# Kernel tuning notes

Hardware: AMD Instinct MI355X
Metric: run time of the kernel (lower is better)

Reference implementation:

```python
import jax, jax.numpy as jnp
import numpy as np

EMBED_DIM = 384
HEADS = 6
HEAD_DIM = EMBED_DIM // HEADS
WINDOW = 64


def setup_inputs() -> dict:
    key = jax.random.key(0)
    ks = jax.random.split(key, 5)
    B, T = 128, 256
    s_attn = 1.0 / np.sqrt(EMBED_DIM)
    x = jax.random.normal(ks[0], (B, T, EMBED_DIM), dtype=jnp.float32)
    W_attn = jax.random.normal(ks[1], (EMBED_DIM, 3 * EMBED_DIM), dtype=jnp.float32) * s_attn
    b_attn = jax.random.normal(ks[2], (3 * EMBED_DIM,), dtype=jnp.float32) * 0.02
    W_proj = jax.random.normal(ks[3], (EMBED_DIM, EMBED_DIM), dtype=jnp.float32) * s_attn
    b_proj = jax.random.normal(ks[4], (EMBED_DIM,), dtype=jnp.float32) * 0.02
    return {"x": x, "W_attn": W_attn, "b_attn": b_attn, "W_proj": W_proj, "b_proj": b_proj}


def reference(x, W_attn, b_attn, W_proj, b_proj):
    B, T, C = x.shape
    qkv = x @ W_attn + b_attn  # [B,T,3C]
    q, k, v = jnp.split(qkv, 3, axis=-1)
    # [B, H, T, hd]
    q = q.reshape(B, T, HEADS, HEAD_DIM).transpose(0, 2, 1, 3)
    k = k.reshape(B, T, HEADS, HEAD_DIM).transpose(0, 2, 1, 3)
    v = v.reshape(B, T, HEADS, HEAD_DIM).transpose(0, 2, 1, 3)
    scale = 1.0 / np.sqrt(HEAD_DIM).astype(np.float32)
    att = jnp.einsum('bhqd,bhkd->bhqk', q, k) * scale
    i = jnp.arange(T)
    causal = i[:, None] >= i[None, :]
    local = jnp.abs(i[:, None] - i[None, :]) <= WINDOW
    mask = (causal & local)[None, None, :, :]
    att = jnp.where(mask, att, -jnp.inf)
    att = jax.nn.softmax(att, axis=-1)
    y = jnp.einsum('bhqk,bhkd->bhqd', att, v)
    y = y.transpose(0, 2, 1, 3).reshape(B, T, C)
    return y @ W_proj + b_proj
```

## Files before the change

kernel.cpp:

```cpp
#include <hip/hip_runtime.h>

#define B_SZ   128
#define T_SEQ  256
#define C_DIM  384
#define HEADS  6
#define HD     64
#define WIN    64

typedef __bf16 bf16x8 __attribute__((ext_vector_type(8)));
typedef float  f32x4  __attribute__((ext_vector_type(4)));

typedef __attribute__((address_space(3))) void lds_void;
typedef __attribute__((address_space(1))) void gbl_void;

__device__ __forceinline__ unsigned short f2bf(float f) {
  unsigned u = __float_as_uint(f);
  u += 0x7FFFu + ((u >> 16) & 1u);
  return (unsigned short)(u >> 16);
}

__global__ __launch_bounds__(256) void convert_f32_bf16(
    const float* __restrict__ in, unsigned short* __restrict__ out, int n4) {
  int i = blockIdx.x * blockDim.x + threadIdx.x;
  if (i < n4) {
    float4 v = ((const float4*)in)[i];
    ushort4 o;
    o.x = f2bf(v.x); o.y = f2bf(v.y); o.z = f2bf(v.z); o.w = f2bf(v.w);
    ((ushort4*)out)[i] = o;
  }
}

__global__ __launch_bounds__(256) void transpose_convert(
    const float* __restrict__ in, unsigned short* __restrict__ out,
    int K, int N) {
  __shared__ float tile[32][33];
  const int gx = blockIdx.x * 32;
  const int gy = blockIdx.y * 32;
  const int tx = threadIdx.x;
  const int ty = threadIdx.y;
#pragma unroll
  for (int r = ty; r < 32; r += 8)
    tile[r][tx] = in[(size_t)(gy + r) * N + gx + tx];
  __syncthreads();
#pragma unroll
  for (int r = ty; r < 32; r += 8)
    out[(size_t)(gx + r) * K + gy + tx] = f2bf(tile[tx][r]);
}

template <bool OUT_BF16>
__global__ __launch_bounds__(256, 2) void gemm_mfma_bf16(
    const unsigned short* __restrict__ A,
    const unsigned short* __restrict__ Bt,
    const float* __restrict__ bias,
    void* __restrict__ Cv, int M, int N, int K, int tiles_n) {
  __shared__ __attribute__((aligned(16))) char smem_raw[48 * 1024];
  unsigned short* As = (unsigned short*)smem_raw;
  unsigned short* Bs = As + 256 * 64;
  float* ep = (float*)smem_raw;

  const int t    = threadIdx.x;
  const int lane = t & 63;
  const int w    = t >> 6;

  const unsigned id    = blockIdx.x;
  const unsigned remap = (id & 7u) * (gridDim.x >> 3) + (id >> 3);
  const int by = remap / (unsigned)tiles_n;
  const int bx = remap % (unsigned)tiles_n;
  const int m0 = by * 256;
  const int n0 = bx * 128;

  const int lrow = lane >> 3;
  const int lcol = lane & 7;
  const int schunk = lcol ^ lrow;

  f32x4 acc[4][8];
#pragma unroll
  for (int i = 0; i < 4; ++i)
#pragma unroll
    for (int j = 0; j < 8; ++j) acc[i][j] = (f32x4){0.f, 0.f, 0.f, 0.f};

  const int mfrag = lane & 15;
  const int quad  = lane >> 4;
  const int sw    = mfrag & 7;

  for (int k0 = 0; k0 < K; k0 += 64) {
#pragma unroll
    for (int i = 0; i < 8; ++i) {
      const int inst = w * 8 + i;
      const int r = inst * 8 + lrow;
      const unsigned short* ga = A + (size_t)(m0 + r) * K + k0 + schunk * 8;
      __builtin_amdgcn_global_load_lds((const gbl_void*)ga,
                                       (lds_void*)(As + inst * 512), 16, 0, 0);
    }
#pragma unroll
    for (int i = 0; i < 4; ++i) {
      const int inst = w * 4 + i;
      const int r = inst * 8 + lrow;
      const unsigned short* gb = Bt + (size_t)(n0 + r) * K + k0 + schunk * 8;
      __builtin_amdgcn_global_load_lds((const gbl_void*)gb,
                                       (lds_void*)(Bs + inst * 512), 16, 0, 0);
    }
    __syncthreads();

#pragma unroll
    for (int ks = 0; ks < 64; ks += 32) {
      const int cp = (((ks >> 3) + quad) ^ sw) << 3;
      bf16x8 af[4], bfr[8];
#pragma unroll
      for (int mt = 0; mt < 4; ++mt)
        af[mt] = *(const bf16x8*)(As + (size_t)(w * 64 + mt * 16 + mfrag) * 64 + cp);
#pragma unroll
      for (int nt = 0; nt < 8; ++nt)
        bfr[nt] = *(const bf16x8*)(Bs + (size_t)(nt * 16 + mfrag) * 64 + cp);
#pragma unroll
      for (int mt = 0; mt < 4; ++mt)
#pragma unroll
        for (int nt = 0; nt < 8; ++nt)
          acc[mt][nt] = __builtin_amdgcn_mfma_f32_16x16x32_bf16(
              af[mt], bfr[nt], acc[mt][nt], 0, 0, 0);
    }
    __syncthreads();
  }

  float bv[8];
#pragma unroll
  for (int nt = 0; nt < 8; ++nt) bv[nt] = bias[n0 + nt * 16 + mfrag];

#pragma unroll
  for (int p = 0; p < 4; ++p) {
    if (p) __syncthreads();
    if (w == p) {
#pragma unroll
      for (int mt = 0; mt < 4; ++mt)
#pragma unroll
        for (int nt = 0; nt < 8; ++nt)
#pragma unroll
          for (int r = 0; r < 4; ++r)
            ep[(mt * 16 + quad * 4 + r) * 132 + nt * 16 + mfrag] =
                acc[mt][nt][r] + bv[nt];
    }
    __syncthreads();
#pragma unroll
    for (int cc = 0; cc < 8; ++cc) {
      const int chunk = cc * 256 + t;
      const int row = chunk >> 5;
      const int c4  = chunk & 31;
      f32x4 v = *(const f32x4*)(ep + row * 132 + c4 * 4);
      const int grow = m0 + p * 64 + row;
      const int gcol = n0 + c4 * 4;
      if (OUT_BF16) {
        ushort4 o;
        o.x = f2bf(v[0]); o.y = f2bf(v[1]); o.z = f2bf(v[2]); o.w = f2bf(v[3]);
        *(ushort4*)((unsigned short*)Cv + (size_t)grow * N + gcol) = o;
      } else {
        *(f32x4*)((float*)Cv + (size_t)grow * N + gcol) = v;
      }
    }
  }
}

#define PSTR 68
__global__ __launch_bounds__(256) void attn_mfma(
    const unsigned short* __restrict__ qkv, unsigned short* __restrict__ y) {
  __shared__ unsigned short Qs[64 * 64];
  __shared__ unsigned short Ks[64 * 64];
  __shared__ unsigned short Vt[64 * 64];
  __shared__ float Pw[4][16 * PSTR];

  const unsigned id  = blockIdx.x;
  const unsigned bid = (id & 7u) * (gridDim.x >> 3) + (id >> 3);
  const int qt  = bid & 3;
  const int h   = (bid >> 2) % HEADS;
  const int b   = bid / (4 * HEADS);
  const int t   = threadIdx.x;
  const int lane = t & 63;
  const int w    = t >> 6;
  const int quad = lane >> 4;
  const int m16  = lane & 15;
  const int sw   = m16 & 7;

  const size_t rowbase = (size_t)b * T_SEQ * (3 * C_DIM);
  const int qoff = h * HD;
  const int koff = C_DIM + h * HD;
  const int voff = 2 * C_DIM + h * HD;
  const int qg0  = qt * 64;

  const int lrow = lane >> 3;
  const int lcol = lane & 7;
  const int schunk = lcol ^ lrow;

#pragma unroll
  for (int i = 0; i < 2; ++i) {
    const int inst = w * 2 + i;
    const int r = inst * 8 + lrow;
    const unsigned short* ga =
        qkv + rowbase + (size_t)(qg0 + r) * (3 * C_DIM) + qoff + schunk * 8;
    __builtin_amdgcn_global_load_lds((const gbl_void*)ga,
                                     (lds_void*)(Qs + inst * 512), 16, 0, 0);
  }

  float m_r[4], l_r[4];
  f32x4 yacc[4];
#pragma unroll
  for (int r = 0; r < 4; ++r) { m_r[r] = -1e30f; l_r[r] = 0.f; }
#pragma unroll
  for (int dt = 0; dt < 4; ++dt) yacc[dt] = (f32x4){0.f, 0.f, 0.f, 0.f};

  const int nchunks  = (qt == 0) ? 1 : 2;
  const int kb_first = (qt == 0) ? 0 : (qg0 - 64);
  const int qrow_base = qg0 + w * 16 + quad * 4;

  for (int ch = 0; ch < nchunks; ++ch) {
    const int kb = kb_first + ch * 64;

    __syncthreads();

#pragma unroll
    for (int i = 0; i < 2; ++i) {
      const int inst = w * 2 + i;
      const int r = inst * 8 + lrow;
      const unsigned short* ga =
          qkv + rowbase + (size_t)(kb + r) * (3 * C_DIM) + koff + schunk * 8;
      __builtin_amdgcn_global_load_lds((const gbl_void*)ga,
                                       (lds_void*)(Ks + inst * 512), 16, 0, 0);
    }
    {
      const int vkey = t & 63;
      const int kc = vkey >> 3, ke = vkey & 7;
      const int vd0  = (t >> 6) * 16;
      const unsigned short* gv =
          qkv + rowbase + (size_t)(kb + vkey) * (3 * C_DIM) + voff + vd0;
#pragma unroll
      for (int u = 0; u < 4; ++u) {
        ushort4 vv = *(const ushort4*)(gv + u * 4);
#pragma unroll
        for (int jj = 0; jj < 4; ++jj) {
          const int d = vd0 + u * 4 + jj;
          const unsigned short val =
              (jj == 0) ? vv.x : (jj == 1) ? vv.y : (jj == 2) ? vv.z : vv.w;
          Vt[d * 64 + ((kc ^ (d & 7)) << 3) + ke] = val;
        }
      }
    }
    __syncthreads();

    f32x4 sacc[4];
#pragma unroll
    for (int nt = 0; nt < 4; ++nt) sacc[nt] = (f32x4){0.f, 0.f, 0.f, 0.f};
#pragma unroll
    for (int ks = 0; ks < 64; ks += 32) {
      const int cp = (((ks >> 3) + quad) ^ sw) << 3;
      bf16x8 aq = *(const bf16x8*)(Qs + (size_t)(w * 16 + m16) * 64 + cp);
#pragma unroll
      for (int nt = 0; nt < 4; ++nt) {
        bf16x8 kf = *(const bf16x8*)(Ks + (size_t)(nt * 16 + m16) * 64 + cp);
        sacc[nt] = __builtin_amdgcn_mfma_f32_16x16x32_bf16(aq, kf, sacc[nt], 0, 0, 0);
      }
    }

    float mc[4] = {-1e30f, -1e30f, -1e30f, -1e30f};
#pragma unroll
    for (int nt = 0; nt < 4; ++nt) {
      const int kg = kb + nt * 16 + m16;
#pragma unroll
      for (int r = 0; r < 4; ++r) {
        const int qg = qrow_base + r;
        const bool valid = (kg <= qg) && (qg - kg <= WIN);
        const float sv = valid ? (sacc[nt][r] * 0.125f) : -1e30f;
        sacc[nt][r] = sv;
        mc[r] = fmaxf(mc[r], sv);
      }
    }
#pragma unroll
    for (int r = 0; r < 4; ++r) {
#pragma unroll
      for (int x = 1; x <= 8; x <<= 1) mc[r] = fmaxf(mc[r], __shfl_xor(mc[r], x));
    }

#pragma unroll
    for (int r = 0; r < 4; ++r) {
      const float mn    = fmaxf(m_r[r], mc[r]);
      const float alpha = __expf(m_r[r] - mn);
      m_r[r] = mn;
      l_r[r] *= alpha;
#pragma unroll
      for (int dt = 0; dt < 4; ++dt) yacc[dt][r] *= alpha;
      float ls = 0.f;
#pragma unroll
      for (int nt = 0; nt < 4; ++nt) {
        const float p = __expf(sacc[nt][r] - mn);
        sacc[nt][r] = p;
        ls += p;
      }
#pragma unroll
      for (int x = 1; x <= 8; x <<= 1) ls += __shfl_xor(ls, x);
      l_r[r] += ls;
    }

#pragma unroll
    for (int nt = 0; nt < 4; ++nt)
#pragma unroll
      for (int r = 0; r < 4; ++r)
        Pw[w][(quad * 4 + r) * PSTR + nt * 16 + m16] = sacc[nt][r];

#pragma unroll
    for (int ks = 0; ks < 64; ks += 32) {
      f32x4 pa = *(const f32x4*)(&Pw[w][m16 * PSTR + ks + quad * 8]);
      f32x4 pb = *(const f32x4*)(&Pw[w][m16 * PSTR + ks + quad * 8 + 4]);
      bf16x8 ap;
#pragma unroll
      for (int j = 0; j < 4; ++j) {
        ap[j]     = (__bf16)pa[j];
        ap[4 + j] = (__bf16)pb[j];
      }
      const int cp = (((ks >> 3) + quad) ^ sw) << 3;
#pragma unroll
      for (int dt = 0; dt < 4; ++dt) {
        bf16x8 vf = *(const bf16x8*)(Vt + (size_t)(dt * 16 + m16) * 64 + cp);
        yacc[dt] = __builtin_amdgcn_mfma_f32_16x16x32_bf16(ap, vf, yacc[dt], 0, 0, 0);
      }
    }
  }

  float* epy = &Pw[0][0];
  float inv[4];
#pragma unroll
  for (int r = 0; r < 4; ++r) inv[r] = 1.f / l_r[r];
#pragma unroll
  for (int dt = 0; dt < 4; ++dt)
#pragma unroll
    for (int r = 0; r < 4; ++r)
      epy[(w * 16 + quad * 4 + r) * PSTR + dt * 16 + m16] = yacc[dt][r] * inv[r];
  __syncthreads();
#pragma unroll
  for (int cc = 0; cc < 4; ++cc) {
    const int chunk = cc * 256 + t;
    const int row = chunk >> 4;
    const int c4  = chunk & 15;
    f32x4 v = *(const f32x4*)(epy + row * PSTR + c4 * 4);
    ushort4 o;
    o.x = f2bf(v[0]); o.y = f2bf(v[1]); o.z = f2bf(v[2]); o.w = f2bf(v[3]);
    *(ushort4*)(y + (size_t)(b * T_SEQ + qg0 + row) * C_DIM + h * HD + c4 * 4) = o;
  }
}

extern "C" void kernel_launch(void* const* d_in, const int* in_sizes, int n_in,
                              void* d_out, int out_size, void* d_ws, size_t ws_size,
                              hipStream_t stream) {
  const float* x      = (const float*)d_in[0];
  const float* W_attn = (const float*)d_in[1];
  const float* b_attn = (const float*)d_in[2];
  const float* W_proj = (const float*)d_in[3];
  const float* b_proj = (const float*)d_in[4];
  float* out = (float*)d_out;

  const int M = B_SZ * T_SEQ;

  unsigned short* qkv_b = (unsigned short*)d_ws;
  unsigned short* y_b   = qkv_b + (size_t)M * (3 * C_DIM);
  unsigned short* x_b   = y_b   + (size_t)M * C_DIM;
  unsigned short* Wa_t  = x_b   + (size_t)M * C_DIM;
  unsigned short* Wp_t  = Wa_t  + (size_t)(3 * C_DIM) * C_DIM;

  {
    int n4 = M * C_DIM / 4;
    convert_f32_bf16<<<n4 / 256, 256, 0, stream>>>(x, x_b, n4);
    transpose_convert<<<dim3((3 * C_DIM) / 32, C_DIM / 32), dim3(32, 8), 0, stream>>>(
        W_attn, Wa_t, C_DIM, 3 * C_DIM);
    transpose_convert<<<dim3(C_DIM / 32, C_DIM / 32), dim3(32, 8), 0, stream>>>(
        W_proj, Wp_t, C_DIM, C_DIM);
  }

  gemm_mfma_bf16<true><<<dim3(9 * (M / 256)), 256, 0, stream>>>(
      x_b, Wa_t, b_attn, qkv_b, M, 3 * C_DIM, C_DIM, 9);

  attn_mfma<<<dim3(B_SZ * HEADS * (T_SEQ / 64)), 256, 0, stream>>>(qkv_b, y_b);

  gemm_mfma_bf16<false><<<dim3(3 * (M / 256)), 256, 0, stream>>>(
      y_b, Wp_t, b_proj, out, M, C_DIM, C_DIM, 3);
}
```

Before: 210.9 us.

## Double-buffer GEMM LDS tiles with smaller 128x128 blocks and higher occupancy

Restructures the bf16 MFMA GEMM from 256x128 tiles with a 64-wide K step to 128x128 tiles with a 32-wide K step. Global-to-LDS loads for the next K slice are issued while the current slice is computed, and warps are arranged 2x2. Smaller tiles and less LDS allow four blocks per CU and more blocks overall, at the cost of lower per-block operand reuse and more loop iterations.

```diff
diff --git a/kernel.cpp b/kernel.cpp
--- a/kernel.cpp
+++ b/kernel.cpp
@@ -48,95 +48,105 @@
 }
 
 template <bool OUT_BF16>
-__global__ __launch_bounds__(256, 2) void gemm_mfma_bf16(
+__global__ __launch_bounds__(256, 4) void gemm_mfma_bf16(
     const unsigned short* __restrict__ A,
     const unsigned short* __restrict__ Bt,
     const float* __restrict__ bias,
     void* __restrict__ Cv, int M, int N, int K, int tiles_n) {
-  __shared__ __attribute__((aligned(16))) char smem_raw[48 * 1024];
-  unsigned short* As = (unsigned short*)smem_raw;
-  unsigned short* Bs = As + 256 * 64;
+  __shared__ __attribute__((aligned(16))) char smem_raw[64 * 132 * 4];
+  unsigned short* As0 = (unsigned short*)smem_raw;
+  unsigned short* Bs0 = As0 + 128 * 32;
+  unsigned short* As1 = Bs0 + 128 * 32;
+  unsigned short* Bs1 = As1 + 128 * 32;
   float* ep = (float*)smem_raw;
 
   const int t    = threadIdx.x;
   const int lane = t & 63;
   const int w    = t >> 6;
+  const int wr   = w >> 1;
+  const int wc   = w & 1;
 
   const unsigned id    = blockIdx.x;
   const unsigned remap = (id & 7u) * (gridDim.x >> 3) + (id >> 3);
   const int by = remap / (unsigned)tiles_n;
   const int bx = remap % (unsigned)tiles_n;
-  const int m0 = by * 256;
+  const int m0 = by * 128;
   const int n0 = bx * 128;
 
-  const int lrow = lane >> 3;
-  const int lcol = lane & 7;
-  const int schunk = lcol ^ lrow;
-
-  f32x4 acc[4][8];
+  const int lrow = lane >> 2;
+  const int lcol = lane & 3;
+  const int sc   = lcol ^ ((lrow >> 1) & 3);
+
+  const int m16  = lane & 15;
+  const int quad = lane >> 4;
+  const int cp   = (quad ^ ((m16 >> 1) & 3)) << 3;
+
+  f32x4 acc[4][4];
 #pragma unroll
   for (int i = 0; i < 4; ++i)
 #pragma unroll
-    for (int j = 0; j < 8; ++j) acc[i][j] = (f32x4){0.f, 0.f, 0.f, 0.f};
-
-  const int mfrag = lane & 15;
-  const int quad  = lane >> 4;
-  const int sw    = mfrag & 7;
-
-  for (int k0 = 0; k0 < K; k0 += 64) {
-#pragma unroll
-    for (int i = 0; i < 8; ++i) {
-      const int inst = w * 8 + i;
-      const int r = inst * 8 + lrow;
-      const unsigned short* ga = A + (size_t)(m0 + r) * K + k0 + schunk * 8;
+    for (int j = 0; j < 4; ++j) acc[i][j] = (f32x4){0.f, 0.f, 0.f, 0.f};
+
+  auto stage = [&](unsigned short* Ad, unsigned short* Bd, int k0) {
+#pragma unroll
+    for (int i = 0; i < 2; ++i) {
+      const int inst = w * 2 + i;
+      const int r = inst * 16 + lrow;
+      const unsigned short* ga = A + (size_t)(m0 + r) * K + k0 + sc * 8;
       __builtin_amdgcn_global_load_lds((const gbl_void*)ga,
-                                       (lds_void*)(As + inst * 512), 16, 0, 0);
-    }
-#pragma unroll
-    for (int i = 0; i < 4; ++i) {
-      const int inst = w * 4 + i;
-      const int r = inst * 8 + lrow;
-      const unsigned short* gb = Bt + (size_t)(n0 + r) * K + k0 + schunk * 8;
+                                       (lds_void*)(Ad + inst * 512), 16, 0, 0);
+    }
+#pragma unroll
+    for (int i = 0; i < 2; ++i) {
+      const int inst = w * 2 + i;
+      const int r = inst * 16 + lrow;
+      const unsigned short* gb = Bt + (size_t)(n0 + r) * K + k0 + sc * 8;
       __builtin_amdgcn_global_load_lds((const gbl_void*)gb,
-                                       (lds_void*)(Bs + inst * 512), 16, 0, 0);
+                                       (lds_void*)(Bd + inst * 512), 16, 0, 0);
+    }
+  };
+
+  const int nk = K >> 5;
+  stage(As0, Bs0, 0);
+  __syncthreads();
+
+  unsigned short *Ac = As0, *Bc = Bs0, *An = As1, *Bn = Bs1;
+  for (int kt = 0; kt < nk; ++kt) {
+    if (kt + 1 < nk) stage(An, Bn, (kt + 1) << 5);
+
+    bf16x8 af[4];
+#pragma unroll
+    for (int mt = 0; mt < 4; ++mt)
+      af[mt] = *(const bf16x8*)(Ac + (size_t)(wr * 64 + mt * 16 + m16) * 32 + cp);
+#pragma unroll
+    for (int nt = 0; nt < 4; ++nt) {
+      bf16x8 bfr = *(const bf16x8*)(Bc + (size_t)(wc * 64 + nt * 16 + m16) * 32 + cp);
+#pragma unroll
+      for (int mt = 0; mt < 4; ++mt)
+        acc[mt][nt] = __builtin_amdgcn_mfma_f32_16x16x32_bf16(
+            af[mt], bfr, acc[mt][nt], 0, 0, 0);
     }
     __syncthreads();
-
-#pragma unroll
-    for (int ks = 0; ks < 64; ks += 32) {
-      const int cp = (((ks >> 3) + quad) ^ sw) << 3;
-      bf16x8 af[4], bfr[8];
+    unsigned short* tp;
+    tp = Ac; Ac = An; An = tp;
+    tp = Bc; Bc = Bn; Bn = tp;
+  }
+
+  float bv[4];
+#pragma unroll
+  for (int nt = 0; nt < 4; ++nt) bv[nt] = bias[n0 + wc * 64 + nt * 16 + m16];
+
+#pragma unroll
+  for (int p = 0; p < 2; ++p) {
+    if (p) __syncthreads();
+    if (wr == p) {
 #pragma unroll
       for (int mt = 0; mt < 4; ++mt)
-        af[mt] = *(const bf16x8*)(As + (size_t)(w * 64 + mt * 16 + mfrag) * 64 + cp);
-#pragma unroll
-      for (int nt = 0; nt < 8; ++nt)
-        bfr[nt] = *(const bf16x8*)(Bs + (size_t)(nt * 16 + mfrag) * 64 + cp);
-#pragma unroll
-      for (int mt = 0; mt < 4; ++mt)
-#pragma unroll
-        for (int nt = 0; nt < 8; ++nt)
-          acc[mt][nt] = __builtin_amdgcn_mfma_f32_16x16x32_bf16(
-              af[mt], bfr[nt], acc[mt][nt], 0, 0, 0);
-    }
-    __syncthreads();
-  }
-
-  float bv[8];
-#pragma unroll
-  for (int nt = 0; nt < 8; ++nt) bv[nt] = bias[n0 + nt * 16 + mfrag];
-
-#pragma unroll
-  for (int p = 0; p < 4; ++p) {
-    if (p) __syncthreads();
-    if (w == p) {
-#pragma unroll
-      for (int mt = 0; mt < 4; ++mt)
-#pragma unroll
-        for (int nt = 0; nt < 8; ++nt)
+#pragma unroll
+        for (int nt = 0; nt < 4; ++nt)
 #pragma unroll
           for (int r = 0; r < 4; ++r)
-            ep[(mt * 16 + quad * 4 + r) * 132 + nt * 16 + mfrag] =
+            ep[(mt * 16 + quad * 4 + r) * 132 + wc * 64 + nt * 16 + m16] =
                 acc[mt][nt][r] + bv[nt];
     }
     __syncthreads();
@@ -371,11 +381,11 @@
         W_proj, Wp_t, C_DIM, C_DIM);
   }
 
-  gemm_mfma_bf16<true><<<dim3(9 * (M / 256)), 256, 0, stream>>>(
+  gemm_mfma_bf16<true><<<dim3(9 * (M / 128)), 256, 0, stream>>>(
       x_b, Wa_t, b_attn, qkv_b, M, 3 * C_DIM, C_DIM, 9);
 
   attn_mfma<<<dim3(B_SZ * HEADS * (T_SEQ / 64)), 256, 0, stream>>>(qkv_b, y_b);
 
-  gemm_mfma_bf16<false><<<dim3(3 * (M / 256)), 256, 0, stream>>>(
+  gemm_mfma_bf16<false><<<dim3(3 * (M / 128)), 256, 0, stream>>>(
       y_b, Wp_t, b_proj, out, M, C_DIM, C_DIM, 3);
 }
```

After: 202.4 us. 4.0% less time.
